# Optimization experiments

Hardware: AMD Instinct MI355X
Metric: run time of the kernel (lower is better)

Reference implementation:

```python
import jax, jax.numpy as jnp
import numpy as np

T, B, D, H, L = 512, 512, 64, 128, 2
Y_LEN = 24


def gru_cell(x, h, Wih, Whh, bih, bhh):
    # PyTorch GRU cell, gate order (r, z, n)
    gi = x @ Wih.T + bih          # [B, 3H]
    gh = h @ Whh.T + bhh          # [B, 3H]
    ir, iz, i_n = jnp.split(gi, 3, axis=-1)
    hr, hz, h_n = jnp.split(gh, 3, axis=-1)
    r = jax.nn.sigmoid(ir + hr)
    z = jax.nn.sigmoid(iz + hz)
    n = jnp.tanh(i_n + r * h_n)
    return (1.0 - z) * n + z * h


def bigru_layer(inp, h0, Wih, Whh, bih, bhh):
    # inp [T,B,in]; Wih [2,3H,in]; Whh [2,3H,H]; bih/bhh [2,3H]; h0 [2,B,H]
    def step_f(h, x):
        h = gru_cell(x, h, Wih[0], Whh[0], bih[0], bhh[0])
        return h, h

    def step_b(h, x):
        h = gru_cell(x, h, Wih[1], Whh[1], bih[1], bhh[1])
        return h, h

    hf, out_f = jax.lax.scan(step_f, h0[0], inp)
    hb, out_b = jax.lax.scan(step_b, h0[1], jnp.flip(inp, 0))
    out_b = jnp.flip(out_b, 0)
    return jnp.concatenate([out_f, out_b], -1), hf, hb


def forward(x, enc_Wih0, enc_Wih1, enc_Whh, enc_bih, enc_bhh,
            dec_Wih0, dec_Wih1, dec_Whh, dec_bih, dec_bhh, fc_w, fc_b):
    batch = x.shape[1]
    # ---- encoder: 2-layer bidirectional GRU, h0 = 0 ----
    layer_in = x
    hn = []
    for l in range(L):
        Wih = enc_Wih0 if l == 0 else enc_Wih1
        h0 = jnp.zeros((2, batch, H), x.dtype)
        layer_in, hf, hb = bigru_layer(layer_in, h0, Wih, enc_Whh[l], enc_bih[l], enc_bhh[l])
        hn += [hf, hb]
    dec_h = jnp.stack(hn)                # [2L, B, H], layer-major (fwd, bwd)
    # dropout on h0 is eval-mode identity
    x0 = x[-1, :, 0:1]                   # [B, 1]

    def step(carry, _):
        xin, h = carry
        lin = xin
        new_h = []
        for l in range(L):
            Wih = dec_Wih0 if l == 0 else dec_Wih1
            hf = gru_cell(lin, h[2 * l],     Wih[0], dec_Whh[l, 0], dec_bih[l, 0], dec_bhh[l, 0])
            hb = gru_cell(lin, h[2 * l + 1], Wih[1], dec_Whh[l, 1], dec_bih[l, 1], dec_bhh[l, 1])
            lin = jnp.concatenate([hf, hb], -1)
            new_h += [hf, hb]
        pred = lin @ fc_w.T + fc_b       # [B, 1]
        return (pred, jnp.stack(new_h)), pred[:, 0]

    _, preds = jax.lax.scan(step, (x0, dec_h), None, length=Y_LEN)
    return preds[..., None]              # [24, B, 1]


def setup_inputs():
    key = jax.random.key(0)
    ks = jax.random.split(key, 13)
    scale = 1.0 / np.sqrt(H).astype(np.float32)
    u = lambda k, shape: jax.random.uniform(k, shape, jnp.float32, -scale, scale)
    return {
        "x": jax.random.normal(ks[0], (T, B, D), jnp.float32),
        "enc_Wih0": u(ks[1], (2, 3 * H, D)),
        "enc_Wih1": u(ks[2], (2, 3 * H, 2 * H)),
        "enc_Whh": u(ks[3], (L, 2, 3 * H, H)),
        "enc_bih": u(ks[4], (L, 2, 3 * H)),
        "enc_bhh": u(ks[5], (L, 2, 3 * H)),
        "dec_Wih0": u(ks[6], (2, 3 * H, 1)),
        "dec_Wih1": u(ks[7], (2, 3 * H, 2 * H)),
        "dec_Whh": u(ks[8], (L, 2, 3 * H, H)),
        "dec_bih": u(ks[9], (L, 2, 3 * H)),
        "dec_bhh": u(ks[10], (L, 2, 3 * H)),
        "fc_w": u(ks[11], (1, 2 * H)),
        "fc_b": u(ks[12], (1,)),
    }


def reference(x, enc_Wih0, enc_Wih1, enc_Whh, enc_bih, enc_bhh,
              dec_Wih0, dec_Wih1, dec_Whh, dec_bih, dec_bhh, fc_w, fc_b):
    return forward(x, enc_Wih0, enc_Wih1, enc_Whh, enc_bih, enc_bhh,
                   dec_Wih0, dec_Wih1, dec_Whh, dec_bih, dec_bhh, fc_w, fc_b)
```

## Files before the change

### kernel.cpp

```cpp
#include <hip/hip_runtime.h>
#include <cstdint>
#include <cstddef>


typedef __attribute__((ext_vector_type(8))) short short8_t;
typedef __attribute__((ext_vector_type(4))) short short4_t;
typedef __attribute__((ext_vector_type(4))) float f32x4_t;

#define MFMA16(a, b, c) __builtin_amdgcn_mfma_f32_16x16x32_bf16((a), (b), (c), 0, 0, 0)

#define BAR_LDS() asm volatile("s_waitcnt lgkmcnt(0)\n\ts_barrier" ::: "memory")

static __device__ __forceinline__ float bf2f(unsigned short u) {
  unsigned int v = ((unsigned int)u) << 16;
  return __builtin_bit_cast(float, v);
}
static __device__ __forceinline__ unsigned short f2bf(float f) {
  unsigned int x = __builtin_bit_cast(unsigned int, f);
  x += 0x7fffu + ((x >> 16) & 1u);
  return (unsigned short)(x >> 16);
}
static __device__ __forceinline__ short8_t ld8(const unsigned short* p) {
  return *reinterpret_cast<const short8_t*>(p);
}
static __device__ __forceinline__ f32x4_t ldf4(const float* p) {
  return *reinterpret_cast<const f32x4_t*>(p);
}
static __device__ __forceinline__ short8_t cvt8f(const float* p) {
  const f32x4_t* v = reinterpret_cast<const f32x4_t*>(p);
  f32x4_t a = v[0], b = v[1];
  short8_t r;
  r[0] = (short)f2bf(a[0]); r[1] = (short)f2bf(a[1]);
  r[2] = (short)f2bf(a[2]); r[3] = (short)f2bf(a[3]);
  r[4] = (short)f2bf(b[0]); r[5] = (short)f2bf(b[1]);
  r[6] = (short)f2bf(b[2]); r[7] = (short)f2bf(b[3]);
  return r;
}
static __device__ __forceinline__ float sigm(float x) { return 1.0f / (1.0f + __expf(-x)); }
static __device__ __forceinline__ float tanh_fast(float y) {
  float t = __expf(-2.0f * fabsf(y));
  float r = (1.0f - t) / (1.0f + t);
  return copysignf(r, y);
}

__global__ void k_prep(const float* __restrict__ x,
                       const float* __restrict__ dWih1, const float* __restrict__ dWhh,
                       unsigned short* __restrict__ bdWih1, unsigned short* __restrict__ bdWhh,
                       float* __restrict__ x0save) {
  const int NW = 24576;
  int i = blockIdx.x * blockDim.x + threadIdx.x;
  if (i < NW) {
    *reinterpret_cast<short8_t*>(bdWih1 + (size_t)i * 8) = cvt8f(dWih1 + (size_t)i * 8);
  } else if (i < 2 * NW) {
    int j = i - NW;
    *reinterpret_cast<short8_t*>(bdWhh + (size_t)j * 8) = cvt8f(dWhh + (size_t)j * 8);
  } else if (i < 2 * NW + 512) {
    int b = i - 2 * NW;
    x0save[b] = x[((size_t)511 * 512 + b) * 64];
  }
}

__global__ void k_copy(const float* __restrict__ x, float* __restrict__ xc,
                       int b_base, int Bc) {
  size_t i = (size_t)blockIdx.x * blockDim.x + threadIdx.x;
  size_t per = (size_t)Bc * 16;
  size_t n = (size_t)512 * per;
  if (i >= n) return;
  size_t t = i / per, r = i - t * per;
  const f32x4_t* s =
      reinterpret_cast<const f32x4_t*>(x + ((size_t)t * 512 + b_base) * 64) + r;
  f32x4_t* d = reinterpret_cast<f32x4_t*>(xc + t * per * 4) + r;
  *d = *s;
}

__global__ __launch_bounds__(256, 1) void k_scan0d(
    float* x,
    float* xc,
    const float* __restrict__ Wih,
    const float* __restrict__ bih,
    const float* __restrict__ Whh,
    const float* __restrict__ bhh,
    float* __restrict__ HS,
    int b_base, int Bc) {
  int dir = blockIdx.y;
  int bl0 = blockIdx.x * 16;
  int b0g = b_base + bl0;
  float* xin = dir ? xc : x;
  unsigned short* yout = (unsigned short*)xin;
  int xstr = dir ? Bc : 512;
  int xb0 = dir ? bl0 : b0g;
  int tid = threadIdx.x, w = tid >> 6, lane = tid & 63, q = lane >> 4, c16 = lane & 15;
  __shared__ unsigned short xl[2][16 * 72];
  __shared__ unsigned short hl[2][16 * 136];
  const float* Wi = Wih + (size_t)dir * 384 * 64;
  const float* Wh = Whh + (size_t)dir * 384 * 128;
  const float* bi = bih + dir * 384;
  const float* bh = bhh + dir * 384;

  short8_t fi[6][2], fh[6][4];
  float brz[4], bni[2], bnh[2];
#pragma unroll
  for (int g = 0; g < 3; g++)
#pragma unroll
    for (int cc = 0; cc < 2; cc++) {
      int f = g * 2 + cc;
      int n0 = g * 128 + w * 32 + cc * 16;
#pragma unroll
      for (int kt = 0; kt < 2; kt++)
        fi[f][kt] = cvt8f(Wi + (size_t)(n0 + c16) * 64 + kt * 32 + q * 8);
#pragma unroll
      for (int kt = 0; kt < 4; kt++)
        fh[f][kt] = cvt8f(Wh + (size_t)(n0 + c16) * 128 + kt * 32 + q * 8);
      if (g < 2) brz[f] = bi[n0 + c16] + bh[n0 + c16];
      else { bni[cc] = bi[n0 + c16]; bnh[cc] = bh[n0 + c16]; }
    }

  float h[2][4];
#pragma unroll
  for (int cc = 0; cc < 2; cc++)
#pragma unroll
    for (int rr = 0; rr < 4; rr++) h[cc][rr] = 0.f;
  for (int i = tid; i < 16 * 136; i += 256) hl[0][i] = 0;

  int srow = tid >> 4, sc = tid & 15;
  {
    int t0 = dir ? 511 : 0;
    f32x4_t v = ldf4(xin + ((size_t)t0 * xstr + xb0 + srow) * 64 + sc * 4);
    unsigned short* dst = &xl[0][srow * 72 + sc * 4];
    dst[0] = f2bf(v[0]); dst[1] = f2bf(v[1]); dst[2] = f2bf(v[2]); dst[3] = f2bf(v[3]);
  }
  f32x4_t pA, pB;
  {
    int t1 = dir ? 510 : 1;
    pA = ldf4(xin + ((size_t)t1 * xstr + xb0 + srow) * 64 + sc * 4);
  }
  __syncthreads();

  auto body = [&](int s, const f32x4_t& xu, f32x4_t& xnl) {
    int cur = s & 1, nxt = cur ^ 1;
    if (s < 510) {
      int tn = dir ? (509 - s) : (s + 2);
      xnl = ldf4(xin + ((size_t)tn * xstr + xb0 + srow) * 64 + sc * 4);
    }
    if (s > 0) {
      int tp = dir ? (512 - s) : (s - 1);
      short8_t v = ld8(&hl[cur][srow * 136 + sc * 8]);
      *reinterpret_cast<short8_t*>(
          yout + ((size_t)tp * xstr + xb0 + srow) * 128 + sc * 8) = v;
    }
    short8_t ax[2], ah[4];
#pragma unroll
    for (int kt = 0; kt < 2; kt++) ax[kt] = ld8(&xl[cur][c16 * 72 + kt * 32 + q * 8]);
#pragma unroll
    for (int kt = 0; kt < 4; kt++) ah[kt] = ld8(&hl[cur][c16 * 136 + kt * 32 + q * 8]);
    f32x4_t aRZ[4], aNi[2], aNh[2];
#pragma unroll
    for (int f = 0; f < 4; f++) aRZ[f] = (f32x4_t){0.f, 0.f, 0.f, 0.f};
#pragma unroll
    for (int cc = 0; cc < 2; cc++) {
      aNi[cc] = (f32x4_t){0.f, 0.f, 0.f, 0.f};
      aNh[cc] = (f32x4_t){0.f, 0.f, 0.f, 0.f};
    }
#pragma unroll
    for (int kt = 0; kt < 2; kt++) {
#pragma unroll
      for (int f = 0; f < 4; f++) aRZ[f] = MFMA16(ax[kt], fi[f][kt], aRZ[f]);
#pragma unroll
      for (int cc = 0; cc < 2; cc++) aNi[cc] = MFMA16(ax[kt], fi[4 + cc][kt], aNi[cc]);
    }
#pragma unroll
    for (int kt = 0; kt < 4; kt++) {
#pragma unroll
      for (int f = 0; f < 4; f++) aRZ[f] = MFMA16(ah[kt], fh[f][kt], aRZ[f]);
#pragma unroll
      for (int cc = 0; cc < 2; cc++) aNh[cc] = MFMA16(ah[kt], fh[4 + cc][kt], aNh[cc]);
    }
#pragma unroll
    for (int cc = 0; cc < 2; cc++)
#pragma unroll
      for (int rr = 0; rr < 4; rr++) {
        float r = sigm(aRZ[cc][rr] + brz[cc]);
        float z = sigm(aRZ[2 + cc][rr] + brz[2 + cc]);
        float n = tanh_fast(aNi[cc][rr] + bni[cc] + r * (aNh[cc][rr] + bnh[cc]));
        float hn = n + z * (h[cc][rr] - n);
        h[cc][rr] = hn;
        hl[nxt][(q * 4 + rr) * 136 + w * 32 + c16 + cc * 16] = f2bf(hn);
      }
    if (s < 511) {
      unsigned short* dst = &xl[nxt][srow * 72 + sc * 4];
      dst[0] = f2bf(xu[0]); dst[1] = f2bf(xu[1]); dst[2] = f2bf(xu[2]); dst[3] = f2bf(xu[3]);
    }
    BAR_LDS();
  };

  for (int s2 = 0; s2 < 256; s2++) {
    body(2 * s2, pA, pB);
    body(2 * s2 + 1, pB, pA);
  }
  {
    int tp = dir ? 0 : 511;
    short8_t v = ld8(&hl[0][srow * 136 + sc * 8]);
    *reinterpret_cast<short8_t*>(
        yout + ((size_t)tp * xstr + xb0 + srow) * 128 + sc * 8) = v;
  }
#pragma unroll
  for (int cc = 0; cc < 2; cc++)
#pragma unroll
    for (int rr = 0; rr < 4; rr++)
      HS[((size_t)dir * 512 + b0g + q * 4 + rr) * 128 + w * 32 + c16 + cc * 16] = h[cc][rr];
}

__global__ __launch_bounds__(512, 1) void k_scan1(
    const unsigned short* __restrict__ OutF,
    const unsigned short* __restrict__ OutB,
    const float* __restrict__ Wih1,
    const float* __restrict__ bih1,
    const float* __restrict__ Whh1,
    const float* __restrict__ bhh1,
    float* __restrict__ HS,
    int b_base, int Bc) {
  int dir = blockIdx.y;
  int b0l = blockIdx.x * 16;
  int tid = threadIdx.x, w = tid >> 6, lane = tid & 63, q = lane >> 4, c16 = lane & 15;
  __shared__ unsigned short il[2][16 * 264];
  __shared__ unsigned short hl[2][16 * 136];
  const float* Wi = Wih1 + (size_t)dir * 384 * 256;
  const float* Wh = Whh1 + (size_t)dir * 384 * 128;
  const float* bi = bih1 + dir * 384;
  const float* bh = bhh1 + dir * 384;

  short8_t fi[3][8], fh[3][4];
  float brz[2], bni, bnh;
#pragma unroll
  for (int g = 0; g < 3; g++) {
    int n0 = g * 128 + w * 16;
#pragma unroll
    for (int kt = 0; kt < 8; kt++)
      fi[g][kt] = cvt8f(Wi + (size_t)(n0 + c16) * 256 + kt * 32 + q * 8);
#pragma unroll
    for (int kt = 0; kt < 4; kt++)
      fh[g][kt] = cvt8f(Wh + (size_t)(n0 + c16) * 128 + kt * 32 + q * 8);
    if (g < 2) brz[g] = bi[n0 + c16] + bh[n0 + c16];
    else { bni = bi[n0 + c16]; bnh = bh[n0 + c16]; }
  }

  float h[4] = {0.f, 0.f, 0.f, 0.f};
  for (int i = tid; i < 16 * 136; i += 512) hl[0][i] = 0;

  int srow = tid >> 5, sc = tid & 31;
  {
    int t0 = dir ? 511 : 0;
    short8_t v = (sc < 16)
        ? ld8(OutF + ((size_t)t0 * 512 + b_base + b0l + srow) * 128 + sc * 8)
        : ld8(OutB + ((size_t)t0 * Bc + b0l + srow) * 128 + (sc - 16) * 8);
    *reinterpret_cast<short8_t*>(&il[0][srow * 264 + sc * 8]) = v;
  }
  short8_t ivA, ivB;
  {
    int t1 = dir ? 510 : 1;
    ivA = (sc < 16)
        ? ld8(OutF + ((size_t)t1 * 512 + b_base + b0l + srow) * 128 + sc * 8)
        : ld8(OutB + ((size_t)t1 * Bc + b0l + srow) * 128 + (sc - 16) * 8);
  }
  __syncthreads();

  auto body = [&](int s, const short8_t& iu, short8_t& inl) {
    int cur = s & 1, nxt = cur ^ 1;
    if (s < 510) {
      int tn = dir ? (509 - s) : (s + 2);
      inl = (sc < 16)
          ? ld8(OutF + ((size_t)tn * 512 + b_base + b0l + srow) * 128 + sc * 8)
          : ld8(OutB + ((size_t)tn * Bc + b0l + srow) * 128 + (sc - 16) * 8);
    }
    f32x4_t aI[3], aH[3];
#pragma unroll
    for (int g = 0; g < 3; g++) {
      aI[g] = (f32x4_t){0.f, 0.f, 0.f, 0.f};
      aH[g] = (f32x4_t){0.f, 0.f, 0.f, 0.f};
    }
#pragma unroll
    for (int kt = 0; kt < 8; kt++) {
      short8_t a = ld8(&il[cur][c16 * 264 + kt * 32 + q * 8]);
#pragma unroll
      for (int g = 0; g < 3; g++) aI[g] = MFMA16(a, fi[g][kt], aI[g]);
    }
#pragma unroll
    for (int kt = 0; kt < 4; kt++) {
      short8_t a = ld8(&hl[cur][c16 * 136 + kt * 32 + q * 8]);
#pragma unroll
      for (int g = 0; g < 3; g++) aH[g] = MFMA16(a, fh[g][kt], aH[g]);
    }
#pragma unroll
    for (int rr = 0; rr < 4; rr++) {
      float r = sigm(aI[0][rr] + aH[0][rr] + brz[0]);
      float z = sigm(aI[1][rr] + aH[1][rr] + brz[1]);
      float n = tanh_fast(aI[2][rr] + bni + r * (aH[2][rr] + bnh));
      float hn = n + z * (h[rr] - n);
      h[rr] = hn;
      hl[nxt][(q * 4 + rr) * 136 + w * 16 + c16] = f2bf(hn);
    }
    if (s < 511)
      *reinterpret_cast<short8_t*>(&il[nxt][srow * 264 + sc * 8]) = iu;
    BAR_LDS();
  };

  for (int s2 = 0; s2 < 256; s2++) {
    body(2 * s2, ivA, ivB);
    body(2 * s2 + 1, ivB, ivA);
  }
#pragma unroll
  for (int rr = 0; rr < 4; rr++)
    HS[((size_t)(2 + dir) * 512 + b_base + b0l + q * 4 + rr) * 128 + w * 16 + c16] = h[rr];
}

__global__ __launch_bounds__(512, 1) void k_dec(
    const float* __restrict__ x0save,
    const float* __restrict__ HS,
    const unsigned short* __restrict__ Whh,
    const unsigned short* __restrict__ Wih1,
    const float* __restrict__ Wih0,
    const float* __restrict__ bih,
    const float* __restrict__ bhh,
    const float* __restrict__ fc_w,
    const float* __restrict__ fcb,
    float* __restrict__ out) {
  int b0 = blockIdx.x * 16;
  int tid = threadIdx.x, w = tid >> 6, lane = tid & 63, q = lane >> 4, c16 = lane & 15;
  int d = w >> 2, w4 = w & 3;
  __shared__ unsigned short hc0[16 * 264];
  __shared__ unsigned short hc1[16 * 264];
  __shared__ float x0s[16];
  __shared__ float fcwf[256];
  int jj = w4 * 32 + c16;
  int jw = w4 * 32;

  const unsigned short* Wd0 = Whh + (size_t)d * 384 * 128;
  const unsigned short* Wh1 = Whh + (size_t)(2 + d) * 384 * 128;
  const unsigned short* Wi1 = Wih1 + (size_t)d * 384 * 256;

  float hs[2][2][4];
#pragma unroll
  for (int l = 0; l < 2; l++)
#pragma unroll
    for (int cc = 0; cc < 2; cc++)
#pragma unroll
      for (int rr = 0; rr < 4; rr++) {
        int row = q * 4 + rr, j = jj + cc * 16;
        int cell = l * 2 + d;
        float v = HS[((size_t)cell * 512 + b0 + row) * 128 + j];
        hs[l][cc][rr] = v;
        unsigned short bv = f2bf(v);
        unsigned short* tile = l ? hc1 : hc0;
        tile[row * 264 + d * 128 + j] = bv;
      }
  if (tid < 16) x0s[tid] = x0save[b0 + tid];
  if (tid < 256) fcwf[tid] = fc_w[tid];

  float w0c[2][3], bi0[2][3], bh0[2][3], bi1[2][3], bh1[2][3];
#pragma unroll
  for (int cc = 0; cc < 2; cc++)
#pragma unroll
    for (int g = 0; g < 3; g++) {
      int col = g * 128 + jj + cc * 16;
      w0c[cc][g] = Wih0[d * 384 + col];
      bi0[cc][g] = bih[d * 384 + col];
      bh0[cc][g] = bhh[d * 384 + col];
      bi1[cc][g] = bih[(2 + d) * 384 + col];
      bh1[cc][g] = bhh[(2 + d) * 384 + col];
    }
  __syncthreads();

  for (int st = 0; st < 24; st++) {
    float hn0[2][4];
    {
      short8_t a0[4];
#pragma unroll
      for (int kt = 0; kt < 4; kt++)
        a0[kt] = ld8(&hc0[c16 * 264 + d * 128 + kt * 32 + q * 8]);
      short8_t w0[24];
#pragma unroll
      for (int kt = 0; kt < 4; kt++)
#pragma unroll
        for (int g = 0; g < 3; g++)
#pragma unroll
          for (int cc = 0; cc < 2; cc++) {
            int n0 = g * 128 + jw + cc * 16;
            w0[kt * 6 + g * 2 + cc] =
                ld8(Wd0 + (size_t)(n0 + c16) * 128 + kt * 32 + q * 8);
          }
      f32x4_t acc[6];
#pragma unroll
      for (int f = 0; f < 6; f++) acc[f] = (f32x4_t){0.f, 0.f, 0.f, 0.f};
#pragma unroll
      for (int kt = 0; kt < 4; kt++)
#pragma unroll
        for (int g = 0; g < 3; g++)
#pragma unroll
          for (int cc = 0; cc < 2; cc++) {
            int f = g * 2 + cc;
            acc[f] = MFMA16(a0[kt], w0[kt * 6 + g * 2 + cc], acc[f]);
          }
#pragma unroll
      for (int cc = 0; cc < 2; cc++)
#pragma unroll
        for (int rr = 0; rr < 4; rr++) {
          float xin = x0s[q * 4 + rr];
          float r = sigm(xin * w0c[cc][0] + bi0[cc][0] + acc[cc][rr] + bh0[cc][0]);
          float z = sigm(xin * w0c[cc][1] + bi0[cc][1] + acc[2 + cc][rr] + bh0[cc][1]);
          float n = tanh_fast(xin * w0c[cc][2] + bi0[cc][2] +
                              r * (acc[4 + cc][rr] + bh0[cc][2]));
          float hv = n + z * (hs[0][cc][rr] - n);
          hn0[cc][rr] = hv;
          hs[0][cc][rr] = hv;
        }
    }
    __syncthreads();
#pragma unroll
    for (int cc = 0; cc < 2; cc++)
#pragma unroll
      for (int rr = 0; rr < 4; rr++)
        hc0[(q * 4 + rr) * 264 + d * 128 + jj + cc * 16] = f2bf(hn0[cc][rr]);
    __syncthreads();

    float hn1[2][4];
    {
      short8_t ai[8];
#pragma unroll
      for (int kt = 0; kt < 8; kt++) ai[kt] = ld8(&hc0[c16 * 264 + kt * 32 + q * 8]);
      short8_t ah[4];
#pragma unroll
      for (int kt = 0; kt < 4; kt++)
        ah[kt] = ld8(&hc1[c16 * 264 + d * 128 + kt * 32 + q * 8]);
      f32x4_t aRZ[4], aNi[2], aNh[2];
#pragma unroll
      for (int f = 0; f < 4; f++) aRZ[f] = (f32x4_t){0.f, 0.f, 0.f, 0.f};
#pragma unroll
      for (int cc = 0; cc < 2; cc++) {
        aNi[cc] = (f32x4_t){0.f, 0.f, 0.f, 0.f};
        aNh[cc] = (f32x4_t){0.f, 0.f, 0.f, 0.f};
      }
      {
        short8_t wA[24];
#pragma unroll
        for (int kt = 0; kt < 4; kt++) {
#pragma unroll
          for (int f = 0; f < 4; f++) {
            int n0 = (f >> 1) * 128 + jw + (f & 1) * 16;
            wA[kt * 6 + f] = ld8(Wi1 + (size_t)(n0 + c16) * 256 + kt * 32 + q * 8);
          }
#pragma unroll
          for (int cc = 0; cc < 2; cc++) {
            int n0 = 256 + jw + cc * 16;
            wA[kt * 6 + 4 + cc] = ld8(Wi1 + (size_t)(n0 + c16) * 256 + kt * 32 + q * 8);
          }
        }
#pragma unroll
        for (int kt = 0; kt < 4; kt++) {
#pragma unroll
          for (int f = 0; f < 4; f++) aRZ[f] = MFMA16(ai[kt], wA[kt * 6 + f], aRZ[f]);
#pragma unroll
          for (int cc = 0; cc < 2; cc++) aNi[cc] = MFMA16(ai[kt], wA[kt * 6 + 4 + cc], aNi[cc]);
        }
      }
      {
        short8_t wB[24];
#pragma unroll
        for (int kt = 0; kt < 4; kt++) {
#pragma unroll
          for (int f = 0; f < 4; f++) {
            int n0 = (f >> 1) * 128 + jw + (f & 1) * 16;
            wB[kt * 6 + f] = ld8(Wi1 + (size_t)(n0 + c16) * 256 + (kt + 4) * 32 + q * 8);
          }
#pragma unroll
          for (int cc = 0; cc < 2; cc++) {
            int n0 = 256 + jw + cc * 16;
            wB[kt * 6 + 4 + cc] = ld8(Wi1 + (size_t)(n0 + c16) * 256 + (kt + 4) * 32 + q * 8);
          }
        }
#pragma unroll
        for (int kt = 0; kt < 4; kt++) {
#pragma unroll
          for (int f = 0; f < 4; f++) aRZ[f] = MFMA16(ai[4 + kt], wB[kt * 6 + f], aRZ[f]);
#pragma unroll
          for (int cc = 0; cc < 2; cc++) aNi[cc] = MFMA16(ai[4 + kt], wB[kt * 6 + 4 + cc], aNi[cc]);
        }
      }
      {
        short8_t wH[24];
#pragma unroll
        for (int kt = 0; kt < 4; kt++) {
#pragma unroll
          for (int f = 0; f < 4; f++) {
            int n0 = (f >> 1) * 128 + jw + (f & 1) * 16;
            wH[kt * 6 + f] = ld8(Wh1 + (size_t)(n0 + c16) * 128 + kt * 32 + q * 8);
          }
#pragma unroll
          for (int cc = 0; cc < 2; cc++) {
            int n0 = 256 + jw + cc * 16;
            wH[kt * 6 + 4 + cc] = ld8(Wh1 + (size_t)(n0 + c16) * 128 + kt * 32 + q * 8);
          }
        }
#pragma unroll
        for (int kt = 0; kt < 4; kt++) {
#pragma unroll
          for (int f = 0; f < 4; f++) aRZ[f] = MFMA16(ah[kt], wH[kt * 6 + f], aRZ[f]);
#pragma unroll
          for (int cc = 0; cc < 2; cc++) aNh[cc] = MFMA16(ah[kt], wH[kt * 6 + 4 + cc], aNh[cc]);
        }
      }
#pragma unroll
      for (int cc = 0; cc < 2; cc++)
#pragma unroll
        for (int rr = 0; rr < 4; rr++) {
          float r = sigm(aRZ[cc][rr] + bi1[cc][0] + bh1[cc][0]);
          float z = sigm(aRZ[2 + cc][rr] + bi1[cc][1] + bh1[cc][1]);
          float n = tanh_fast(aNi[cc][rr] + bi1[cc][2] + r * (aNh[cc][rr] + bh1[cc][2]));
          float hv = n + z * (hs[1][cc][rr] - n);
          hn1[cc][rr] = hv;
          hs[1][cc][rr] = hv;
        }
    }
    __syncthreads();
#pragma unroll
    for (int cc = 0; cc < 2; cc++)
#pragma unroll
      for (int rr = 0; rr < 4; rr++)
        hc1[(q * 4 + rr) * 264 + d * 128 + jj + cc * 16] = f2bf(hn1[cc][rr]);
    __syncthreads();

    if (w == 0) {
      float s = 0.f;
#pragma unroll
      for (int i = 0; i < 8; i++) {
        short8_t hv = ld8(&hc1[c16 * 264 + q * 64 + i * 8]);
#pragma unroll
        for (int e = 0; e < 8; e++)
          s += bf2f((unsigned short)hv[e]) * fcwf[q * 64 + i * 8 + e];
      }
      s += __shfl_xor(s, 16);
      s += __shfl_xor(s, 32);
      if (q == 0) {
        float pred = s + fcb[0];
        x0s[c16] = pred;
        out[(size_t)st * 512 + b0 + c16] = pred;
      }
    }
    __syncthreads();
  }
}

extern "C" void kernel_launch(void* const* d_in, const int* in_sizes, int n_in,
                              void* d_out, int out_size, void* d_ws, size_t ws_size,
                              hipStream_t stream) {
  const float* x     = (const float*)d_in[0];
  const float* eWih0 = (const float*)d_in[1];
  const float* eWih1 = (const float*)d_in[2];
  const float* eWhh  = (const float*)d_in[3];
  const float* ebih  = (const float*)d_in[4];
  const float* ebhh  = (const float*)d_in[5];
  const float* dWih0 = (const float*)d_in[6];
  const float* dWih1 = (const float*)d_in[7];
  const float* dWhh  = (const float*)d_in[8];
  const float* dbih  = (const float*)d_in[9];
  const float* dbhh  = (const float*)d_in[10];
  const float* fc_w  = (const float*)d_in[11];
  const float* fc_b  = (const float*)d_in[12];
  float* out = (float*)d_out;
  (void)in_sizes; (void)n_in; (void)out_size;

  const size_t fixedB = 2048 + 1048576 + 393216 + 393216 + 4096;
  int Bc = 256;
  if (fixedB + (size_t)512 * 131072 <= ws_size) Bc = 512;

  char* ws = (char*)d_ws;
  size_t off = 0;
  auto alloc = [&](size_t bytes) -> char* {
    off = (off + 255) & ~(size_t)255;
    char* p = ws + off;
    off += bytes;
    return p;
  };
  float* x0save          = (float*)alloc(2048);
  float* HS              = (float*)alloc(1048576);
  unsigned short* bdWih1 = (unsigned short*)alloc(393216);
  unsigned short* bdWhh  = (unsigned short*)alloc(393216);
  float* xc              = (float*)alloc((size_t)Bc * 131072);

  k_prep<<<194, 256, 0, stream>>>(x, dWih1, dWhh, bdWih1, bdWhh, x0save);

  float* xm = (float*)d_in[0];
  const float* Whh1 = eWhh + (size_t)2 * 384 * 128;
  int nchunks = 512 / Bc;
  for (int c = 0; c < nchunks; c++) {
    int b_base = c * Bc;
    int ncopy = (512 * Bc * 16 + 255) / 256;
    k_copy<<<ncopy, 256, 0, stream>>>(x, xc, b_base, Bc);
    k_scan0d<<<dim3(Bc / 16, 2), 256, 0, stream>>>(xm, xc, eWih0, ebih, eWhh, ebhh,
                                                   HS, b_base, Bc);
    k_scan1<<<dim3(Bc / 16, 2), 512, 0, stream>>>((const unsigned short*)xm,
                                                  (const unsigned short*)xc,
                                                  eWih1, ebih + 768, Whh1,
                                                  ebhh + 768, HS, b_base, Bc);
  }
  k_dec<<<dim3(32), 512, 0, stream>>>(x0save, HS, bdWhh, bdWih1, dWih0, dbih, dbhh,
                                      fc_w, fc_b, out);
}
```

Measured before the change: 2.057 ms.

## Software-pipeline input-projection MFMAs one step ahead in encoder scans; use fast rcp

In both encoder scan kernels, the input-to-hidden matmul for the next timestep is now computed during the current step. It runs after the recurrent matmul and before the gate math, so it is off the serial h-dependency chain. Input staging moves to a deeper prefetch, with tiles two steps ahead in LDS and global loads three steps ahead. Sigmoid and tanh now use the hardware reciprocal instead of a full division. This adds accumulator registers for the double-buffered projections, which may raise register pressure, and the approximate reciprocal slightly changes numerics.

```diff
diff --git a/kernel.cpp b/kernel.cpp
--- a/kernel.cpp
+++ b/kernel.cpp
@@ -36,10 +36,15 @@
   r[6] = (short)f2bf(b[2]); r[7] = (short)f2bf(b[3]);
   return r;
 }
-static __device__ __forceinline__ float sigm(float x) { return 1.0f / (1.0f + __expf(-x)); }
+static __device__ __forceinline__ float frcp(float x) {
+  return __builtin_amdgcn_rcpf(x);
+}
+static __device__ __forceinline__ float sigm(float x) {
+  return frcp(1.0f + __expf(-x));
+}
 static __device__ __forceinline__ float tanh_fast(float y) {
   float t = __expf(-2.0f * fabsf(y));
-  float r = (1.0f - t) / (1.0f + t);
+  float r = (1.0f - t) * frcp(1.0f + t);
   return copysignf(r, y);
 }
 
@@ -123,24 +128,43 @@
   for (int i = tid; i < 16 * 136; i += 256) hl[0][i] = 0;
 
   int srow = tid >> 4, sc = tid & 15;
-  {
-    int t0 = dir ? 511 : 0;
-    f32x4_t v = ldf4(xin + ((size_t)t0 * xstr + xb0 + srow) * 64 + sc * 4);
-    unsigned short* dst = &xl[0][srow * 72 + sc * 4];
+#pragma unroll
+  for (int k = 0; k < 2; k++) {
+    int tk = dir ? (511 - k) : k;
+    f32x4_t v = ldf4(xin + ((size_t)tk * xstr + xb0 + srow) * 64 + sc * 4);
+    unsigned short* dst = &xl[k][srow * 72 + sc * 4];
     dst[0] = f2bf(v[0]); dst[1] = f2bf(v[1]); dst[2] = f2bf(v[2]); dst[3] = f2bf(v[3]);
   }
   f32x4_t pA, pB;
   {
-    int t1 = dir ? 510 : 1;
-    pA = ldf4(xin + ((size_t)t1 * xstr + xb0 + srow) * 64 + sc * 4);
+    int t2 = dir ? 509 : 2;
+    pA = ldf4(xin + ((size_t)t2 * xstr + xb0 + srow) * 64 + sc * 4);
   }
   __syncthreads();
 
-  auto body = [&](int s, const f32x4_t& xu, f32x4_t& xnl) {
+  f32x4_t gxA[6], gxB[6];
+#pragma unroll
+  for (int f = 0; f < 6; f++) gxA[f] = (f32x4_t){0.f, 0.f, 0.f, 0.f};
+#pragma unroll
+  for (int kt = 0; kt < 2; kt++) {
+    short8_t ax = ld8(&xl[0][c16 * 72 + kt * 32 + q * 8]);
+#pragma unroll
+    for (int f = 0; f < 4; f++) gxA[f] = MFMA16(ax, fi[f][kt], gxA[f]);
+#pragma unroll
+    for (int cc = 0; cc < 2; cc++) gxA[4 + cc] = MFMA16(ax, fi[4 + cc][kt], gxA[4 + cc]);
+  }
+  BAR_LDS();
+
+  auto body = [&](int s, f32x4_t (&gxC)[6], f32x4_t (&gxN)[6],
+                  const f32x4_t& xu, f32x4_t& xnl) {
     int cur = s & 1, nxt = cur ^ 1;
+    if (s < 509) {
+      int tn = dir ? (508 - s) : (s + 3);
+      xnl = ldf4(xin + ((size_t)tn * xstr + xb0 + srow) * 64 + sc * 4);
+    }
     if (s < 510) {
-      int tn = dir ? (509 - s) : (s + 2);
-      xnl = ldf4(xin + ((size_t)tn * xstr + xb0 + srow) * 64 + sc * 4);
+      unsigned short* dst = &xl[cur][srow * 72 + sc * 4];
+      dst[0] = f2bf(xu[0]); dst[1] = f2bf(xu[1]); dst[2] = f2bf(xu[2]); dst[3] = f2bf(xu[3]);
     }
     if (s > 0) {
       int tp = dir ? (512 - s) : (s - 1);
@@ -148,54 +172,50 @@
       *reinterpret_cast<short8_t*>(
           yout + ((size_t)tp * xstr + xb0 + srow) * 128 + sc * 8) = v;
     }
-    short8_t ax[2], ah[4];
-#pragma unroll
-    for (int kt = 0; kt < 2; kt++) ax[kt] = ld8(&xl[cur][c16 * 72 + kt * 32 + q * 8]);
+    short8_t ah[4];
 #pragma unroll
     for (int kt = 0; kt < 4; kt++) ah[kt] = ld8(&hl[cur][c16 * 136 + kt * 32 + q * 8]);
-    f32x4_t aRZ[4], aNi[2], aNh[2];
-#pragma unroll
-    for (int f = 0; f < 4; f++) aRZ[f] = (f32x4_t){0.f, 0.f, 0.f, 0.f};
-#pragma unroll
-    for (int cc = 0; cc < 2; cc++) {
-      aNi[cc] = (f32x4_t){0.f, 0.f, 0.f, 0.f};
-      aNh[cc] = (f32x4_t){0.f, 0.f, 0.f, 0.f};
-    }
-#pragma unroll
-    for (int kt = 0; kt < 2; kt++) {
-#pragma unroll
-      for (int f = 0; f < 4; f++) aRZ[f] = MFMA16(ax[kt], fi[f][kt], aRZ[f]);
-#pragma unroll
-      for (int cc = 0; cc < 2; cc++) aNi[cc] = MFMA16(ax[kt], fi[4 + cc][kt], aNi[cc]);
-    }
+    f32x4_t aRZh[4], aNh[2];
+#pragma unroll
+    for (int f = 0; f < 4; f++) aRZh[f] = (f32x4_t){0.f, 0.f, 0.f, 0.f};
+#pragma unroll
+    for (int cc = 0; cc < 2; cc++) aNh[cc] = (f32x4_t){0.f, 0.f, 0.f, 0.f};
 #pragma unroll
     for (int kt = 0; kt < 4; kt++) {
 #pragma unroll
-      for (int f = 0; f < 4; f++) aRZ[f] = MFMA16(ah[kt], fh[f][kt], aRZ[f]);
+      for (int f = 0; f < 4; f++) aRZh[f] = MFMA16(ah[kt], fh[f][kt], aRZh[f]);
 #pragma unroll
       for (int cc = 0; cc < 2; cc++) aNh[cc] = MFMA16(ah[kt], fh[4 + cc][kt], aNh[cc]);
     }
+    if (s < 511) {
+#pragma unroll
+      for (int f = 0; f < 6; f++) gxN[f] = (f32x4_t){0.f, 0.f, 0.f, 0.f};
+#pragma unroll
+      for (int kt = 0; kt < 2; kt++) {
+        short8_t ax = ld8(&xl[nxt][c16 * 72 + kt * 32 + q * 8]);
+#pragma unroll
+        for (int f = 0; f < 4; f++) gxN[f] = MFMA16(ax, fi[f][kt], gxN[f]);
+#pragma unroll
+        for (int cc = 0; cc < 2; cc++) gxN[4 + cc] = MFMA16(ax, fi[4 + cc][kt], gxN[4 + cc]);
+      }
+    }
 #pragma unroll
     for (int cc = 0; cc < 2; cc++)
 #pragma unroll
       for (int rr = 0; rr < 4; rr++) {
-        float r = sigm(aRZ[cc][rr] + brz[cc]);
-        float z = sigm(aRZ[2 + cc][rr] + brz[2 + cc]);
-        float n = tanh_fast(aNi[cc][rr] + bni[cc] + r * (aNh[cc][rr] + bnh[cc]));
+        float r = sigm(gxC[cc][rr] + aRZh[cc][rr] + brz[cc]);
+        float z = sigm(gxC[2 + cc][rr] + aRZh[2 + cc][rr] + brz[2 + cc]);
+        float n = tanh_fast(gxC[4 + cc][rr] + bni[cc] + r * (aNh[cc][rr] + bnh[cc]));
         float hn = n + z * (h[cc][rr] - n);
         h[cc][rr] = hn;
         hl[nxt][(q * 4 + rr) * 136 + w * 32 + c16 + cc * 16] = f2bf(hn);
       }
-    if (s < 511) {
-      unsigned short* dst = &xl[nxt][srow * 72 + sc * 4];
-      dst[0] = f2bf(xu[0]); dst[1] = f2bf(xu[1]); dst[2] = f2bf(xu[2]); dst[3] = f2bf(xu[3]);
-    }
     BAR_LDS();
   };
 
   for (int s2 = 0; s2 < 256; s2++) {
-    body(2 * s2, pA, pB);
-    body(2 * s2 + 1, pB, pA);
+    body(2 * s2, gxA, gxB, pA, pB);
+    body(2 * s2 + 1, gxB, gxA, pB, pA);
   }
   {
     int tp = dir ? 0 : 511;
@@ -248,65 +268,79 @@
   for (int i = tid; i < 16 * 136; i += 512) hl[0][i] = 0;
 
   int srow = tid >> 5, sc = tid & 31;
-  {
-    int t0 = dir ? 511 : 0;
+#pragma unroll
+  for (int k = 0; k < 2; k++) {
+    int tk = dir ? (511 - k) : k;
     short8_t v = (sc < 16)
-        ? ld8(OutF + ((size_t)t0 * 512 + b_base + b0l + srow) * 128 + sc * 8)
-        : ld8(OutB + ((size_t)t0 * Bc + b0l + srow) * 128 + (sc - 16) * 8);
-    *reinterpret_cast<short8_t*>(&il[0][srow * 264 + sc * 8]) = v;
+        ? ld8(OutF + ((size_t)tk * 512 + b_base + b0l + srow) * 128 + sc * 8)
+        : ld8(OutB + ((size_t)tk * Bc + b0l + srow) * 128 + (sc - 16) * 8);
+    *reinterpret_cast<short8_t*>(&il[k][srow * 264 + sc * 8]) = v;
   }
   short8_t ivA, ivB;
   {
-    int t1 = dir ? 510 : 1;
+    int t2 = dir ? 509 : 2;
     ivA = (sc < 16)
-        ? ld8(OutF + ((size_t)t1 * 512 + b_base + b0l + srow) * 128 + sc * 8)
-        : ld8(OutB + ((size_t)t1 * Bc + b0l + srow) * 128 + (sc - 16) * 8);
+        ? ld8(OutF + ((size_t)t2 * 512 + b_base + b0l + srow) * 128 + sc * 8)
+        : ld8(OutB + ((size_t)t2 * Bc + b0l + srow) * 128 + (sc - 16) * 8);
   }
   __syncthreads();
 
-  auto body = [&](int s, const short8_t& iu, short8_t& inl) {
+  f32x4_t giA[3], giB[3];
+#pragma unroll
+  for (int g = 0; g < 3; g++) giA[g] = (f32x4_t){0.f, 0.f, 0.f, 0.f};
+#pragma unroll
+  for (int kt = 0; kt < 8; kt++) {
+    short8_t a = ld8(&il[0][c16 * 264 + kt * 32 + q * 8]);
+#pragma unroll
+    for (int g = 0; g < 3; g++) giA[g] = MFMA16(a, fi[g][kt], giA[g]);
+  }
+  BAR_LDS();
+
+  auto body = [&](int s, f32x4_t (&giC)[3], f32x4_t (&giN)[3],
+                  const short8_t& iu, short8_t& inl) {
     int cur = s & 1, nxt = cur ^ 1;
-    if (s < 510) {
-      int tn = dir ? (509 - s) : (s + 2);
+    if (s < 509) {
+      int tn = dir ? (508 - s) : (s + 3);
       inl = (sc < 16)
           ? ld8(OutF + ((size_t)tn * 512 + b_base + b0l + srow) * 128 + sc * 8)
           : ld8(OutB + ((size_t)tn * Bc + b0l + srow) * 128 + (sc - 16) * 8);
     }
-    f32x4_t aI[3], aH[3];
-#pragma unroll
-    for (int g = 0; g < 3; g++) {
-      aI[g] = (f32x4_t){0.f, 0.f, 0.f, 0.f};
-      aH[g] = (f32x4_t){0.f, 0.f, 0.f, 0.f};
-    }
-#pragma unroll
-    for (int kt = 0; kt < 8; kt++) {
-      short8_t a = ld8(&il[cur][c16 * 264 + kt * 32 + q * 8]);
-#pragma unroll
-      for (int g = 0; g < 3; g++) aI[g] = MFMA16(a, fi[g][kt], aI[g]);
-    }
+    if (s < 510)
+      *reinterpret_cast<short8_t*>(&il[cur][srow * 264 + sc * 8]) = iu;
+    f32x4_t aH[3];
+#pragma unroll
+    for (int g = 0; g < 3; g++) aH[g] = (f32x4_t){0.f, 0.f, 0.f, 0.f};
 #pragma unroll
     for (int kt = 0; kt < 4; kt++) {
       short8_t a = ld8(&hl[cur][c16 * 136 + kt * 32 + q * 8]);
 #pragma unroll
       for (int g = 0; g < 3; g++) aH[g] = MFMA16(a, fh[g][kt], aH[g]);
     }
+    if (s < 511) {
+#pragma unroll
+      for (int g = 0; g < 3; g++) giN[g] = (f32x4_t){0.f, 0.f, 0.f, 0.f};
+#pragma unroll
+      for (int kt = 0; kt < 8; kt++) {
+        short8_t a = ld8(&il[nxt][c16 * 264 + kt * 32 + q * 8]);
+#pragma unroll
+        for (int g = 0; g < 3; g++) giN[g] = MFMA16(a, fi[g][kt], giN[g]);
+      }
+    }
 #pragma unroll
     for (int rr = 0; rr < 4; rr++) {
-      float r = sigm(aI[0][rr] + aH[0][rr] + brz[0]);
-      float z = sigm(aI[1][rr] + aH[1][rr] + brz[1]);
-      float n = tanh_fast(aI[2][rr] + bni + r * (aH[2][rr] + bnh));
+      float r = sigm(giC[0][rr] + aH[0][rr] + brz[0]);
+      float z = sigm(giC[1][rr] + aH[1][rr] + brz[1]);
+      float n = tanh_fast(giC[2][rr] + bni + r * (aH[2][rr] + bnh));
       float hn = n + z * (h[rr] - n);
       h[rr] = hn;
       hl[nxt][(q * 4 + rr) * 136 + w * 16 + c16] = f2bf(hn);
     }
-    if (s < 511)
-      *reinterpret_cast<short8_t*>(&il[nxt][srow * 264 + sc * 8]) = iu;
     BAR_LDS();
   };
 
   for (int s2 = 0; s2 < 256; s2++) {
-    body(2 * s2, ivA, ivB);
-    body(2 * s2 + 1, ivB, ivA);
+    body(2 * s2, giA, giB, ivA, ivB);
+    body(2 * s2 + 1, giB, giA, ivB, ivA);
   }
 #pragma unroll
   for (int rr = 0; rr < 4; rr++)
```

New measurement: 1.750 ms. 1.18x faster.
